# Kernel tuning notes

Measured on AMD Instinct MI355X. Metric: run time of the kernel, lower is better.

## Reference

```python
import jax, jax.numpy as jnp
import numpy as np

LN_EPS = 1e-5


def setup_inputs() -> dict:
    key = jax.random.key(0)
    k1, k2, k3, k4 = jax.random.split(key, 4)
    b, n, d, o, m = 64, 196, 768, 196, 2
    return {
        "x": jax.random.normal(k1, (b, n, d), dtype=jnp.float32),
        "ln_w": jnp.ones((d,), dtype=jnp.float32),
        "ln_b": jnp.zeros((d,), dtype=jnp.float32),
        "sw": jax.random.normal(k2, (o, m, n), dtype=jnp.float32),
        "sb": jax.random.normal(k3, (o, m, n), dtype=jnp.float32),
        "dw": jax.random.normal(k4, (o, m), dtype=jnp.float32),
    }


def reference(x, ln_w, ln_b, sw, sb, dw):
    # LayerNorm over last dim (dim=768)
    mu = jnp.mean(x, axis=-1, keepdims=True)
    var = jnp.mean(jnp.square(x - mu), axis=-1, keepdims=True)
    y = (x - mu) * jax.lax.rsqrt(var + LN_EPS) * ln_w + ln_b  # (b, n, d)

    # Original: repeat y to (b,d,o,m,n), apply sw*y+sb, sum over n.
    # With no synapse activation / dropout this is exactly a contraction:
    # s[b,d,o,m] = sum_n sw[o,m,n]*y[b,n,d] + sum_n sb[o,m,n]
    s = jnp.einsum('bnd,omn->bdom', y, sw) + jnp.sum(sb, axis=-1)  # (b,d,o,m)

    # dendritic weighting then sum over branches m
    t = jnp.sum(dw * s, axis=-1)  # (b, d, o)

    # soma = nn.GELU (exact erf form)
    out = jax.nn.gelu(t, approximate=False)

    out = jnp.transpose(out, (0, 2, 1))  # (b, o, d) == (b, n, d)
    return x * (out + 1.0)
```

## Files before the change

kernel.cpp:

```cpp
#include <hip/hip_runtime.h>
#include <math.h>


#define B_   64
#define N_   196
#define D_   768
#define KQ   7
#define OPAD 256

typedef __attribute__((ext_vector_type(8))) short bf16x8;
typedef __attribute__((ext_vector_type(4))) float f32x4;

__device__ __forceinline__ unsigned short bf16_rne(float f) {
    unsigned u = __builtin_bit_cast(unsigned, f);
    u += 0x7FFFu + ((u >> 16) & 1u);
    return (unsigned short)(u >> 16);
}
__device__ __forceinline__ float bf16_to_f(unsigned short h) {
    unsigned u = ((unsigned)h) << 16;
    return __builtin_bit_cast(float, u);
}

__global__ void prep_w_kernel(const float* __restrict__ sw,
                              const float* __restrict__ sb,
                              const float* __restrict__ dw,
                              unsigned short* __restrict__ Wfh,
                              unsigned short* __restrict__ Wfl,
                              float* __restrict__ rowsum,
                              float* __restrict__ cvec) {
    int o = blockIdx.x;
    int t = threadIdx.x;
    float w0 = 0.f, w1 = 0.f;
    if (o < N_) { w0 = dw[o * 2 + 0]; w1 = dw[o * 2 + 1]; }
    float val = 0.f, sbp = 0.f;
    if (o < N_ && t < N_) {
        val = w0 * sw[(o * 2 + 0) * N_ + t] + w1 * sw[(o * 2 + 1) * N_ + t];
        sbp = w0 * sb[(o * 2 + 0) * N_ + t] + w1 * sb[(o * 2 + 1) * N_ + t];
    }
    if (t < KQ * 32) {
        unsigned short h = bf16_rne(val);
        int addr = ((((o >> 4) * KQ + (t >> 5)) * 4 + ((t >> 3) & 3)) * 16 + (o & 15)) * 8 + (t & 7);
        Wfh[addr] = h;
        Wfl[addr] = bf16_rne(val - bf16_to_f(h));
    }
    __shared__ float r1[256], r2[256];
    r1[t] = val; r2[t] = sbp;
    __syncthreads();
    for (int s = 128; s > 0; s >>= 1) {
        if (t < s) { r1[t] += r1[t + s]; r2[t] += r2[t + s]; }
        __syncthreads();
    }
    if (t == 0) { rowsum[o] = r1[0]; cvec[o] = r2[0]; }
}

__global__ void ln_stats_kernel(const float* __restrict__ x,
                                float* __restrict__ mu,
                                float* __restrict__ rstd) {
    int wave = threadIdx.x >> 6;
    int lane = threadIdx.x & 63;
    int row  = blockIdx.x * 4 + wave;
    const float4* xr = reinterpret_cast<const float4*>(x + (size_t)row * D_);
    float4 v0 = xr[lane];
    float4 v1 = xr[lane + 64];
    float4 v2 = xr[lane + 128];
    float s = v0.x + v0.y + v0.z + v0.w
            + v1.x + v1.y + v1.z + v1.w
            + v2.x + v2.y + v2.z + v2.w;
    #pragma unroll
    for (int off = 32; off >= 1; off >>= 1) s += __shfl_xor(s, off);
    float m = s * (1.0f / D_);
    float q = 0.f;
    {
        float d;
        d = v0.x - m; q += d * d;  d = v0.y - m; q += d * d;
        d = v0.z - m; q += d * d;  d = v0.w - m; q += d * d;
        d = v1.x - m; q += d * d;  d = v1.y - m; q += d * d;
        d = v1.z - m; q += d * d;  d = v1.w - m; q += d * d;
        d = v2.x - m; q += d * d;  d = v2.y - m; q += d * d;
        d = v2.z - m; q += d * d;  d = v2.w - m; q += d * d;
    }
    #pragma unroll
    for (int off = 32; off >= 1; off >>= 1) q += __shfl_xor(q, off);
    if (lane == 0) {
        mu[row]   = m;
        rstd[row] = rsqrtf(q * (1.0f / D_) + 1e-5f);
    }
}


#define LOADC(s, c) do {                                                      \
    _Pragma("unroll")                                                         \
    for (int e = 0; e < 4; ++e) {                                             \
        const int k = (c) * 32 + w * 4 + e;                                   \
        if (k < N_) {                                                         \
            xv[s][e]  = xb[(size_t)k * D_ + d0 + lane];                       \
            mus[s][e] = mub[k];                                               \
            rss[s][e] = rsb[k];                                               \
        } else { xv[s][e] = 0.f; mus[s][e] = 0.f; rss[s][e] = 0.f; }          \
    } } while (0)

#define WRITEC(s) do {                                                        \
    short4 hv, lv; short* hp = &hv.x; short* lp = &lv.x;                      \
    _Pragma("unroll")                                                         \
    for (int e = 0; e < 4; ++e) {                                             \
        float v = (xv[s][e] - mus[s][e]) * rss[s][e];                         \
        unsigned short h = bf16_rne(v);                                       \
        hp[e] = (short)h;                                                     \
        lp[e] = (short)bf16_rne(v - bf16_to_f(h));                            \
    }                                                                         \
    const int ea = ((w >> 1) * 64 + lane) * 8 + (w & 1) * 4;                  \
    *reinterpret_cast<short4*>(&BsH[s][ea]) = hv;                             \
    *reinterpret_cast<short4*>(&BsL[s][ea]) = lv; } while (0)

#define LOADA(slot, c) do {                                                   \
    _Pragma("unroll")                                                         \
    for (int mf = 0; mf < 2; ++mf) {                                          \
        const size_t ab = ((size_t)((w * 2 + mf) * KQ + (c)) * 512) + lane * 8;\
        ah[slot][mf] = *reinterpret_cast<const bf16x8*>(Wfh + ab);            \
        al[slot][mf] = *reinterpret_cast<const bf16x8*>(Wfl + ab);            \
    } } while (0)

__global__ __launch_bounds__(512, 4) void gemm_mfma_kernel(
    const float* __restrict__ x,
    const float* __restrict__ ln_w,
    const float* __restrict__ ln_b,
    const unsigned short* __restrict__ Wfh,
    const unsigned short* __restrict__ Wfl,
    const float* __restrict__ rowsum,
    const float* __restrict__ cvec,
    const float* __restrict__ mu,
    const float* __restrict__ rstd,
    float* __restrict__ out) {
    const int b  = blockIdx.y;
    const int d0 = blockIdx.x * 64;
    const int t = threadIdx.x;
    const int w = t >> 6, lane = t & 63;
    const int m16 = lane & 15, g = lane >> 4;

    __shared__ __align__(16) unsigned short BsH[2][2048];
    __shared__ __align__(16) unsigned short BsL[2][2048];

    const float* xb  = x + (size_t)b * (N_ * D_);
    const float* mub = mu + b * N_;
    const float* rsb = rstd + b * N_;

    float xv[2][4], mus[2][4], rss[2][4];
    bf16x8 ah[2][2], al[2][2];

    f32x4 acc[2][4];
    #pragma unroll
    for (int i = 0; i < 2; ++i)
        #pragma unroll
        for (int j = 0; j < 4; ++j)
            acc[i][j] = (f32x4){0.f, 0.f, 0.f, 0.f};

    LOADC(0, 0);
    LOADC(1, 1);
    LOADA(0, 0);
    WRITEC(0);
    __syncthreads();

    #pragma unroll
    for (int c = 0; c < KQ; ++c) {
        const int s = c & 1;
        if (c > 0) {
            WRITEC(s);
            __syncthreads();
        }
        if (c + 2 < KQ) LOADC(s, c + 2);
        if (c + 1 < KQ) LOADA((c + 1) & 1, c + 1);
        #pragma unroll
        for (int nf = 0; nf < 4; ++nf) {
            const int ba = (g * 64 + nf * 16 + m16) * 8;
            bf16x8 bh = *reinterpret_cast<const bf16x8*>(&BsH[s][ba]);
            bf16x8 bl = *reinterpret_cast<const bf16x8*>(&BsL[s][ba]);
            #pragma unroll
            for (int mf = 0; mf < 2; ++mf) {
                acc[mf][nf] = __builtin_amdgcn_mfma_f32_16x16x32_bf16(ah[s][mf], bh, acc[mf][nf], 0, 0, 0);
                acc[mf][nf] = __builtin_amdgcn_mfma_f32_16x16x32_bf16(ah[s][mf], bl, acc[mf][nf], 0, 0, 0);
                acc[mf][nf] = __builtin_amdgcn_mfma_f32_16x16x32_bf16(al[s][mf], bh, acc[mf][nf], 0, 0, 0);
            }
        }
    }

    float lwv[4], lbv[4];
    #pragma unroll
    for (int nf = 0; nf < 4; ++nf) {
        lwv[nf] = ln_w[d0 + nf * 16 + m16];
        lbv[nf] = ln_b[d0 + nf * 16 + m16];
    }
    #pragma unroll
    for (int mf = 0; mf < 2; ++mf) {
        #pragma unroll
        for (int r = 0; r < 4; ++r) {
            const int o = w * 32 + mf * 16 + g * 4 + r;
            if (o < N_) {
                const float rs = rowsum[o], cc = cvec[o];
                #pragma unroll
                for (int nf = 0; nf < 4; ++nf) {
                    const int d = d0 + nf * 16 + m16;
                    float T = fmaf(lwv[nf], acc[mf][nf][r], fmaf(lbv[nf], rs, cc));
                    float gl = 0.5f * T * (1.0f + erff(T * 0.70710678118654752f));
                    out[((size_t)(b * N_ + o)) * D_ + d] = xb[(size_t)o * D_ + d] * (gl + 1.0f);
                }
            }
        }
    }
}

extern "C" void kernel_launch(void* const* d_in, const int* in_sizes, int n_in,
                              void* d_out, int out_size, void* d_ws, size_t ws_size,
                              hipStream_t stream) {
    const float* x    = (const float*)d_in[0];
    const float* ln_w = (const float*)d_in[1];
    const float* ln_b = (const float*)d_in[2];
    const float* sw   = (const float*)d_in[3];
    const float* sb   = (const float*)d_in[4];
    const float* dw   = (const float*)d_in[5];
    float* out = (float*)d_out;

    float* wsf = (float*)d_ws;
    float* mu     = wsf;
    float* rstd   = mu + B_ * N_;
    float* rowsum = rstd + B_ * N_;
    float* cvec   = rowsum + OPAD;
    unsigned short* Wfh = (unsigned short*)(cvec + OPAD);
    unsigned short* Wfl = Wfh + OPAD * (KQ * 32);

    prep_w_kernel<<<OPAD, 256, 0, stream>>>(sw, sb, dw, Wfh, Wfl, rowsum, cvec);
    ln_stats_kernel<<<(B_ * N_) / 4, 256, 0, stream>>>(x, mu, rstd);
    gemm_mfma_kernel<<<dim3(12, B_), 512, 0, stream>>>(
        x, ln_w, ln_b, Wfh, Wfl, rowsum, cvec, mu, rstd, out);
}
```

Measured before the change: 54.82 us.

## Drop LDS staging; each wave normalizes x directly into MFMA B fragments

The GEMM kernel no longer stages normalized x through shared memory with double buffering and barriers. Each wave now loads x columns straight from global memory, normalizes and splits them into bf16 hi/lo in registers, and feeds them into MFMA. The grid is retiled to 13 output-row tiles by 3 d-groups with 256-thread blocks, giving more blocks with smaller per-wave accumulators. The cost is that x is reloaded and renormalized once for every output tile (13x redundancy), and the global loads are strided by D, in exchange for removing LDS traffic and synchronization.

Measured after the change: 85.78 us. 56.5% more time.

```diff
diff --git a/kernel.cpp b/kernel.cpp
--- a/kernel.cpp
+++ b/kernel.cpp
@@ -39,7 +39,8 @@
     }
     if (t < KQ * 32) {
         unsigned short h = bf16_rne(val);
-        int addr = ((((o >> 4) * KQ + (t >> 5)) * 4 + ((t >> 3) & 3)) * 16 + (o & 15)) * 8 + (t & 7);
+        int addr = (((o >> 4) * KQ + (t >> 5)) * 4 + ((t >> 3) & 3)) * 128
+                 + (o & 15) * 8 + (t & 7);
         Wfh[addr] = h;
         Wfl[addr] = bf16_rne(val - bf16_to_f(h));
     }
@@ -87,40 +88,7 @@
     }
 }
 
-
-#define LOADC(s, c) do {                                                      \
-    _Pragma("unroll")                                                         \
-    for (int e = 0; e < 4; ++e) {                                             \
-        const int k = (c) * 32 + w * 4 + e;                                   \
-        if (k < N_) {                                                         \
-            xv[s][e]  = xb[(size_t)k * D_ + d0 + lane];                       \
-            mus[s][e] = mub[k];                                               \
-            rss[s][e] = rsb[k];                                               \
-        } else { xv[s][e] = 0.f; mus[s][e] = 0.f; rss[s][e] = 0.f; }          \
-    } } while (0)
-
-#define WRITEC(s) do {                                                        \
-    short4 hv, lv; short* hp = &hv.x; short* lp = &lv.x;                      \
-    _Pragma("unroll")                                                         \
-    for (int e = 0; e < 4; ++e) {                                             \
-        float v = (xv[s][e] - mus[s][e]) * rss[s][e];                         \
-        unsigned short h = bf16_rne(v);                                       \
-        hp[e] = (short)h;                                                     \
-        lp[e] = (short)bf16_rne(v - bf16_to_f(h));                            \
-    }                                                                         \
-    const int ea = ((w >> 1) * 64 + lane) * 8 + (w & 1) * 4;                  \
-    *reinterpret_cast<short4*>(&BsH[s][ea]) = hv;                             \
-    *reinterpret_cast<short4*>(&BsL[s][ea]) = lv; } while (0)
-
-#define LOADA(slot, c) do {                                                   \
-    _Pragma("unroll")                                                         \
-    for (int mf = 0; mf < 2; ++mf) {                                          \
-        const size_t ab = ((size_t)((w * 2 + mf) * KQ + (c)) * 512) + lane * 8;\
-        ah[slot][mf] = *reinterpret_cast<const bf16x8*>(Wfh + ab);            \
-        al[slot][mf] = *reinterpret_cast<const bf16x8*>(Wfl + ab);            \
-    } } while (0)
-
-__global__ __launch_bounds__(512, 4) void gemm_mfma_kernel(
+__global__ __launch_bounds__(256, 2) void gemm_mfma_kernel(
     const float* __restrict__ x,
     const float* __restrict__ ln_w,
     const float* __restrict__ ln_b,
@@ -132,54 +100,62 @@
     const float* __restrict__ rstd,
     float* __restrict__ out) {
     const int b  = blockIdx.y;
-    const int d0 = blockIdx.x * 64;
+    const int ot = blockIdx.x % 13;
+    const int dg = blockIdx.x / 13;
     const int t = threadIdx.x;
     const int w = t >> 6, lane = t & 63;
     const int m16 = lane & 15, g = lane >> 4;
-
-    __shared__ __align__(16) unsigned short BsH[2][2048];
-    __shared__ __align__(16) unsigned short BsL[2][2048];
+    const int d0 = dg * 256 + w * 64;
 
     const float* xb  = x + (size_t)b * (N_ * D_);
     const float* mub = mu + b * N_;
     const float* rsb = rstd + b * N_;
 
-    float xv[2][4], mus[2][4], rss[2][4];
-    bf16x8 ah[2][2], al[2][2];
-
-    f32x4 acc[2][4];
-    #pragma unroll
-    for (int i = 0; i < 2; ++i)
-        #pragma unroll
-        for (int j = 0; j < 4; ++j)
-            acc[i][j] = (f32x4){0.f, 0.f, 0.f, 0.f};
-
-    LOADC(0, 0);
-    LOADC(1, 1);
-    LOADA(0, 0);
-    WRITEC(0);
-    __syncthreads();
+    f32x4 acc[4];
+    #pragma unroll
+    for (int j = 0; j < 4; ++j) acc[j] = (f32x4){0.f, 0.f, 0.f, 0.f};
 
     #pragma unroll
     for (int c = 0; c < KQ; ++c) {
-        const int s = c & 1;
-        if (c > 0) {
-            WRITEC(s);
-            __syncthreads();
+        float a_[8], off_[8];
+        if (c < 6 || g == 0) {
+            const int kb = c * 32 + g * 8;
+            float4 m0 = *reinterpret_cast<const float4*>(mub + kb);
+            float4 m1 = *reinterpret_cast<const float4*>(mub + kb + 4);
+            float4 r0 = *reinterpret_cast<const float4*>(rsb + kb);
+            float4 r1 = *reinterpret_cast<const float4*>(rsb + kb + 4);
+            a_[0]=r0.x; a_[1]=r0.y; a_[2]=r0.z; a_[3]=r0.w;
+            a_[4]=r1.x; a_[5]=r1.y; a_[6]=r1.z; a_[7]=r1.w;
+            off_[0]=-m0.x*r0.x; off_[1]=-m0.y*r0.y; off_[2]=-m0.z*r0.z; off_[3]=-m0.w*r0.w;
+            off_[4]=-m1.x*r1.x; off_[5]=-m1.y*r1.y; off_[6]=-m1.z*r1.z; off_[7]=-m1.w*r1.w;
+        } else {
+            #pragma unroll
+            for (int e = 0; e < 8; ++e) { a_[e] = 0.f; off_[e] = 0.f; }
         }
-        if (c + 2 < KQ) LOADC(s, c + 2);
-        if (c + 1 < KQ) LOADA((c + 1) & 1, c + 1);
+        const size_t ab = ((size_t)(ot * KQ + c) * 4 + g) * 128 + m16 * 8;
+        bf16x8 ah = *reinterpret_cast<const bf16x8*>(Wfh + ab);
+        bf16x8 al = *reinterpret_cast<const bf16x8*>(Wfl + ab);
         #pragma unroll
         for (int nf = 0; nf < 4; ++nf) {
-            const int ba = (g * 64 + nf * 16 + m16) * 8;
-            bf16x8 bh = *reinterpret_cast<const bf16x8*>(&BsH[s][ba]);
-            bf16x8 bl = *reinterpret_cast<const bf16x8*>(&BsL[s][ba]);
-            #pragma unroll
-            for (int mf = 0; mf < 2; ++mf) {
-                acc[mf][nf] = __builtin_amdgcn_mfma_f32_16x16x32_bf16(ah[s][mf], bh, acc[mf][nf], 0, 0, 0);
-                acc[mf][nf] = __builtin_amdgcn_mfma_f32_16x16x32_bf16(ah[s][mf], bl, acc[mf][nf], 0, 0, 0);
-                acc[mf][nf] = __builtin_amdgcn_mfma_f32_16x16x32_bf16(al[s][mf], bh, acc[mf][nf], 0, 0, 0);
+            const int d = d0 + nf * 16 + m16;
+            const float* xp = xb + (size_t)(c * 32 + g * 8) * D_ + d;
+            float xv[8];
+            #pragma unroll
+            for (int e = 0; e < 8; ++e) {
+                bool kv = (c < 6) || (g == 0 && e < 4);
+                xv[e] = kv ? xp[(size_t)e * D_] : 0.f;
             }
+            bf16x8 bh, bl;
+            #pragma unroll
+            for (int e = 0; e < 8; ++e) {
+                float v = fmaf(xv[e], a_[e], (c < 6 || (g == 0 && e < 4)) ? off_[e] : 0.f);
+                unsigned short h = bf16_rne(v);
+                bh[e] = (short)h;
+                bl[e] = (short)bf16_rne(v - bf16_to_f(h));
+            }
+            acc[nf] = __builtin_amdgcn_mfma_f32_16x16x32_bf16(ah, bh, acc[nf], 0, 0, 0);
+            acc[nf] = __builtin_amdgcn_mfma_f32_16x16x32_bf16(ah, bl, acc[nf], 0, 0, 0);
+            acc[nf] = __builtin_amdgcn_mfma_f32_16x16x32_bf16(al, bh, acc[nf], 0, 0, 0);
         }
     }
 
@@ -190,19 +166,16 @@
         lbv[nf] = ln_b[d0 + nf * 16 + m16];
     }
     #pragma unroll
-    for (int mf = 0; mf < 2; ++mf) {
-        #pragma unroll
-        for (int r = 0; r < 4; ++r) {
-            const int o = w * 32 + mf * 16 + g * 4 + r;
-            if (o < N_) {
-                const float rs = rowsum[o], cc = cvec[o];
-                #pragma unroll
-                for (int nf = 0; nf < 4; ++nf) {
-                    const int d = d0 + nf * 16 + m16;
-                    float T = fmaf(lwv[nf], acc[mf][nf][r], fmaf(lbv[nf], rs, cc));
-                    float gl = 0.5f * T * (1.0f + erff(T * 0.70710678118654752f));
-                    out[((size_t)(b * N_ + o)) * D_ + d] = xb[(size_t)o * D_ + d] * (gl + 1.0f);
-                }
+    for (int r = 0; r < 4; ++r) {
+        const int o = ot * 16 + g * 4 + r;
+        if (o < N_) {
+            const float rs = rowsum[o], cc = cvec[o];
+            #pragma unroll
+            for (int nf = 0; nf < 4; ++nf) {
+                const int d = d0 + nf * 16 + m16;
+                float T = fmaf(lwv[nf], acc[nf][r], fmaf(lbv[nf], rs, cc));
+                float gl = 0.5f * T * (1.0f + erff(T * 0.70710678118654752f));
+                out[((size_t)(b * N_ + o)) * D_ + d] = xb[(size_t)o * D_ + d] * (gl + 1.0f);
             }
         }
     }
@@ -221,14 +194,14 @@
 
     float* wsf = (float*)d_ws;
     float* mu     = wsf;
-    float* rstd   = mu + B_ * N_;
-    float* rowsum = rstd + B_ * N_;
+    float* rstd   = mu + 12608;
+    float* rowsum = rstd + 12608;
     float* cvec   = rowsum + OPAD;
     unsigned short* Wfh = (unsigned short*)(cvec + OPAD);
-    unsigned short* Wfl = Wfh + OPAD * (KQ * 32);
+    unsigned short* Wfl = Wfh + (OPAD / 16) * KQ * 512;
 
     prep_w_kernel<<<OPAD, 256, 0, stream>>>(sw, sb, dw, Wfh, Wfl, rowsum, cvec);
     ln_stats_kernel<<<(B_ * N_) / 4, 256, 0, stream>>>(x, mu, rstd);
-    gemm_mfma_kernel<<<dim3(12, B_), 512, 0, stream>>>(
+    gemm_mfma_kernel<<<dim3(39, B_), 256, 0, stream>>>(
         x, ln_w, ln_b, Wfh, Wfl, rowsum, cvec, mu, rstd, out);
 }
```

## Precompute normalized split-bf16 B operand in MFMA-ready layout before GEMM

Applied to the files above, without the earlier changes.

Adds a kernel that computes LayerNorm stats, normalizes x, and writes hi/lo bf16 splits to a global buffer packed in k-octets that match the MFMA operand layout. The GEMM then loads B fragments straight from global memory without LDS staging or double buffering, and the old LDS GEMM path is kept as a fallback when workspace is too small. This removes the per-tile conversion and LDS traffic in the GEMM, but adds a full write and re-read of a 2x bf16 copy of x. Variance is now computed in one pass as E[x^2]-mu^2, which is less numerically robust.

After: 55.34 us. Within noise of the previous version (+1.0%).

```diff
diff --git a/kernel.cpp b/kernel.cpp
--- a/kernel.cpp
+++ b/kernel.cpp
@@ -6,6 +6,7 @@
 #define N_   196
 #define D_   768
 #define KQ   7
+#define NKO  28
 #define OPAD 256
 
 typedef __attribute__((ext_vector_type(8))) short bf16x8;
@@ -39,7 +40,8 @@
     }
     if (t < KQ * 32) {
         unsigned short h = bf16_rne(val);
-        int addr = ((((o >> 4) * KQ + (t >> 5)) * 4 + ((t >> 3) & 3)) * 16 + (o & 15)) * 8 + (t & 7);
+        int addr = (((o >> 4) * KQ + (t >> 5)) * 4 + ((t >> 3) & 3)) * 128
+                 + (o & 15) * 8 + (t & 7);
         Wfh[addr] = h;
         Wfl[addr] = bf16_rne(val - bf16_to_f(h));
     }
@@ -51,6 +53,150 @@
         __syncthreads();
     }
     if (t == 0) { rowsum[o] = r1[0]; cvec[o] = r2[0]; }
+}
+
+__global__ __launch_bounds__(512) void ln_split_kernel(
+    const float* __restrict__ x,
+    const float* __restrict__ ln_w,
+    unsigned short* __restrict__ Bh,
+    unsigned short* __restrict__ Bl) {
+    const int koct = blockIdx.x, b = blockIdx.y;
+    const int t = threadIdx.x, w = t >> 6, lane = t & 63;
+    const int k = koct * 8 + w;
+    __shared__ float xs[8][768];
+
+    float4 v0 = make_float4(0.f, 0.f, 0.f, 0.f);
+    float4 v1 = v0, v2 = v0;
+    if (k < N_) {
+        const float4* xr = reinterpret_cast<const float4*>(x + ((size_t)b * N_ + k) * D_);
+        v0 = xr[lane]; v1 = xr[lane + 64]; v2 = xr[lane + 128];
+    }
+    float s = v0.x + v0.y + v0.z + v0.w
+            + v1.x + v1.y + v1.z + v1.w
+            + v2.x + v2.y + v2.z + v2.w;
+    float q = v0.x*v0.x + v0.y*v0.y + v0.z*v0.z + v0.w*v0.w
+            + v1.x*v1.x + v1.y*v1.y + v1.z*v1.z + v1.w*v1.w
+            + v2.x*v2.x + v2.y*v2.y + v2.z*v2.z + v2.w*v2.w;
+    #pragma unroll
+    for (int off = 32; off >= 1; off >>= 1) {
+        s += __shfl_xor(s, off);
+        q += __shfl_xor(q, off);
+    }
+    const float mu   = s * (1.0f / D_);
+    const float var  = q * (1.0f / D_) - mu * mu;
+    const float rstd = rsqrtf(var + 1e-5f);
+
+    const float4* lw4 = reinterpret_cast<const float4*>(ln_w);
+    float4 w0 = lw4[lane], w1 = lw4[lane + 64], w2 = lw4[lane + 128];
+    float4 o0, o1, o2;
+    o0.x = (v0.x - mu) * rstd * w0.x;  o0.y = (v0.y - mu) * rstd * w0.y;
+    o0.z = (v0.z - mu) * rstd * w0.z;  o0.w = (v0.w - mu) * rstd * w0.w;
+    o1.x = (v1.x - mu) * rstd * w1.x;  o1.y = (v1.y - mu) * rstd * w1.y;
+    o1.z = (v1.z - mu) * rstd * w1.z;  o1.w = (v1.w - mu) * rstd * w1.w;
+    o2.x = (v2.x - mu) * rstd * w2.x;  o2.y = (v2.y - mu) * rstd * w2.y;
+    o2.z = (v2.z - mu) * rstd * w2.z;  o2.w = (v2.w - mu) * rstd * w2.w;
+    *reinterpret_cast<float4*>(&xs[w][lane * 4])       = o0;
+    *reinterpret_cast<float4*>(&xs[w][lane * 4 + 256]) = o1;
+    *reinterpret_cast<float4*>(&xs[w][lane * 4 + 512]) = o2;
+    __syncthreads();
+
+    for (int d = t; d < D_; d += 512) {
+        bf16x8 hv, lv;
+        #pragma unroll
+        for (int kk = 0; kk < 8; ++kk) {
+            float v = xs[kk][d];
+            unsigned short h = bf16_rne(v);
+            hv[kk] = (short)h;
+            lv[kk] = (short)bf16_rne(v - bf16_to_f(h));
+        }
+        const size_t base = (((size_t)b * NKO + koct) * D_ + d) * 8;
+        *reinterpret_cast<bf16x8*>(Bh + base) = hv;
+        *reinterpret_cast<bf16x8*>(Bl + base) = lv;
+    }
+}
+
+__global__ __launch_bounds__(512, 4) void gemm_bpk_kernel(
+    const float* __restrict__ x,
+    const float* __restrict__ ln_b,
+    const unsigned short* __restrict__ Wfh,
+    const unsigned short* __restrict__ Wfl,
+    const unsigned short* __restrict__ Bh,
+    const unsigned short* __restrict__ Bl,
+    const float* __restrict__ rowsum,
+    const float* __restrict__ cvec,
+    float* __restrict__ out) {
+    const int b  = blockIdx.y;
+    const int d0 = blockIdx.x * 64;
+    const int t = threadIdx.x;
+    const int w = t >> 6, lane = t & 63;
+    const int m16 = lane & 15, g = lane >> 4;
+
+    const float* xb = x + (size_t)b * (N_ * D_);
+
+    f32x4 acc[2][4];
+    #pragma unroll
+    for (int i = 0; i < 2; ++i)
+        #pragma unroll
+        for (int j = 0; j < 4; ++j)
+            acc[i][j] = (f32x4){0.f, 0.f, 0.f, 0.f};
+
+    #pragma unroll
+    for (int c = 0; c < KQ; ++c) {
+        bf16x8 ah[2], al[2], bh[4], bl[4];
+        const size_t krow = ((size_t)b * NKO + c * 4 + g) * D_;
+        #pragma unroll
+        for (int nf = 0; nf < 4; ++nf) {
+            const size_t e = (krow + d0 + nf * 16 + m16) * 8;
+            bh[nf] = *reinterpret_cast<const bf16x8*>(Bh + e);
+            bl[nf] = *reinterpret_cast<const bf16x8*>(Bl + e);
+        }
+        #pragma unroll
+        for (int mf = 0; mf < 2; ++mf) {
+            const size_t ab = ((size_t)((w * 2 + mf) * KQ + c)) * 512 + lane * 8;
+            ah[mf] = *reinterpret_cast<const bf16x8*>(Wfh + ab);
+            al[mf] = *reinterpret_cast<const bf16x8*>(Wfl + ab);
+        }
+        #pragma unroll
+        for (int nf = 0; nf < 4; ++nf) {
+            #pragma unroll
+            for (int mf = 0; mf < 2; ++mf) {
+                acc[mf][nf] = __builtin_amdgcn_mfma_f32_16x16x32_bf16(ah[mf], bh[nf], acc[mf][nf], 0, 0, 0);
+                acc[mf][nf] = __builtin_amdgcn_mfma_f32_16x16x32_bf16(ah[mf], bl[nf], acc[mf][nf], 0, 0, 0);
+                acc[mf][nf] = __builtin_amdgcn_mfma_f32_16x16x32_bf16(al[mf], bh[nf], acc[mf][nf], 0, 0, 0);
+            }
+        }
+    }
+
+    float lbv[4];
+    #pragma unroll
+    for (int nf = 0; nf < 4; ++nf) lbv[nf] = ln_b[d0 + nf * 16 + m16];
+    #pragma unroll
+    for (int mf = 0; mf < 2; ++mf) {
+        const int obase = (w * 2 + mf) * 16 + g * 4;
+        f32x4 rs4 = *reinterpret_cast<const f32x4*>(rowsum + obase);
+        f32x4 cc4 = *reinterpret_cast<const f32x4*>(cvec + obase);
+        float xres[4][4];
+        #pragma unroll
+        for (int r = 0; r < 4; ++r) {
+            const int o = obase + r;
+            #pragma unroll
+            for (int nf = 0; nf < 4; ++nf)
+                xres[r][nf] = (o < N_) ? xb[(size_t)o * D_ + d0 + nf * 16 + m16] : 0.f;
+        }
+        #pragma unroll
+        for (int r = 0; r < 4; ++r) {
+            const int o = obase + r;
+            if (o < N_) {
+                #pragma unroll
+                for (int nf = 0; nf < 4; ++nf) {
+                    const int d = d0 + nf * 16 + m16;
+                    float T = acc[mf][nf][r] + fmaf(lbv[nf], rs4[r], cc4[r]);
+                    float gl = 0.5f * T * (1.0f + erff(T * 0.70710678118654752f));
+                    out[((size_t)(b * N_ + o)) * D_ + d] = xres[r][nf] * (gl + 1.0f);
+                }
+            }
+        }
+    }
 }
 
 __global__ void ln_stats_kernel(const float* __restrict__ x,
@@ -87,7 +233,6 @@
     }
 }
 
-
 #define LOADC(s, c) do {                                                      \
     _Pragma("unroll")                                                         \
     for (int e = 0; e < 4; ++e) {                                             \
@@ -120,7 +265,7 @@
         al[slot][mf] = *reinterpret_cast<const bf16x8*>(Wfl + ab);            \
     } } while (0)
 
-__global__ __launch_bounds__(512, 4) void gemm_mfma_kernel(
+__global__ __launch_bounds__(512, 4) void gemm_lds_kernel(
     const float* __restrict__ x,
     const float* __restrict__ ln_w,
     const float* __restrict__ ln_b,
@@ -220,15 +365,28 @@
     float* out = (float*)d_out;
 
     float* wsf = (float*)d_ws;
-    float* mu     = wsf;
-    float* rstd   = mu + B_ * N_;
-    float* rowsum = rstd + B_ * N_;
+    float* rowsum = wsf;
     float* cvec   = rowsum + OPAD;
     unsigned short* Wfh = (unsigned short*)(cvec + OPAD);
     unsigned short* Wfl = Wfh + OPAD * (KQ * 32);
+    char* after = (char*)(Wfl + OPAD * (KQ * 32));
+
+    const size_t bpk_elems = (size_t)B_ * NKO * D_ * 8;
+    const size_t need = (size_t)(after - (char*)d_ws) + 2 * bpk_elems * sizeof(unsigned short);
 
     prep_w_kernel<<<OPAD, 256, 0, stream>>>(sw, sb, dw, Wfh, Wfl, rowsum, cvec);
-    ln_stats_kernel<<<(B_ * N_) / 4, 256, 0, stream>>>(x, mu, rstd);
-    gemm_mfma_kernel<<<dim3(12, B_), 512, 0, stream>>>(
-        x, ln_w, ln_b, Wfh, Wfl, rowsum, cvec, mu, rstd, out);
-}
+
+    if (ws_size >= need) {
+        unsigned short* Bh = (unsigned short*)after;
+        unsigned short* Bl = Bh + bpk_elems;
+        ln_split_kernel<<<dim3(NKO, B_), 512, 0, stream>>>(x, ln_w, Bh, Bl);
+        gemm_bpk_kernel<<<dim3(12, B_), 512, 0, stream>>>(
+            x, ln_b, Wfh, Wfl, Bh, Bl, rowsum, cvec, out);
+    } else {
+        float* mu   = (float*)after;
+        float* rstd = mu + 12608;
+        ln_stats_kernel<<<(B_ * N_) / 4, 256, 0, stream>>>(x, mu, rstd);
+        gemm_lds_kernel<<<dim3(12, B_), 512, 0, stream>>>(
+            x, ln_w, ln_b, Wfh, Wfl, rowsum, cvec, mu, rstd, out);
+    }
+}
```
